# Kernel optimization log

Hardware: AMD Instinct MI355X
Metric: run time of the kernel (lower is better)

The kernel has to match this reference:

```python
import jax, jax.numpy as jnp
import numpy as np

K_SIZE = 3
SCALE = 4
PADDING = K_SIZE // 2


def setup_inputs() -> dict:
    key = jax.random.key(0)
    k1, k2, k3, k4 = jax.random.split(key, 4)
    B, C, H, W = 8, 3, 1024, 1024
    ho, wo = H // SCALE, W // SCALE
    img = jax.random.normal(k1, (B, C, H, W), dtype=jnp.float32)
    kernels = jax.random.uniform(k2, (B, K_SIZE * K_SIZE, ho, wo), dtype=jnp.float32)
    offsets_h = jax.random.normal(k3, (B, K_SIZE * K_SIZE, ho, wo), dtype=jnp.float32)
    offsets_v = jax.random.normal(k4, (B, K_SIZE * K_SIZE, ho, wo), dtype=jnp.float32)
    offset_unit = jnp.full((1,), 4.0, dtype=jnp.float32)
    return {"img": img, "kernels": kernels, "offsets_h": offsets_h,
            "offsets_v": offsets_v, "offset_unit": offset_unit}


def _adaptive_downsample(img, kernels, offsets_h, offsets_v, offset_unit):
    # img: [B,C,H,W]; kernels/offsets: [B,k^2,ho,wo]; offset_unit: [1]
    B, C, H, W = img.shape
    ho, wo = kernels.shape[2], kernels.shape[3]
    # reflection pad as in nn.ReflectionPad2d(padding)
    imgp = jnp.pad(img, ((0, 0), (0, 0), (PADDING, PADDING), (PADDING, PADDING)), mode="reflect")
    Hp, Wp = imgp.shape[2], imgp.shape[3]

    k = jnp.arange(K_SIZE)
    ky = jnp.repeat(k, K_SIZE).astype(jnp.float32)  # [k^2] row index of kernel tap
    kx = jnp.tile(k, K_SIZE).astype(jnp.float32)    # [k^2] col index of kernel tap

    # output-pixel centers in original image coords; +PADDING shift into padded
    # coords cancels the -PADDING tap centering, so padded sample position is
    # center + k (k in 0..k_size-1).
    cy = (jnp.arange(ho, dtype=jnp.float32) + 0.5) * SCALE - 0.5  # [ho]
    cx = (jnp.arange(wo, dtype=jnp.float32) + 0.5) * SCALE - 0.5  # [wo]

    ou = offset_unit.reshape(())
    # sample positions in padded image, shape [B, k^2, ho, wo]
    p_y = cy[None, None, :, None] + ky[None, :, None, None] + offsets_v * ou
    p_x = cx[None, None, None, :] + kx[None, :, None, None] + offsets_h * ou

    y0f = jnp.floor(p_y)
    x0f = jnp.floor(p_x)
    beta = p_y - y0f   # vertical bilinear weight
    alpha = p_x - x0f  # horizontal bilinear weight

    y0 = jnp.clip(y0f.astype(jnp.int32), 0, Hp - 1)
    y1 = jnp.clip(y0 + 1, 0, Hp - 1)
    x0 = jnp.clip(x0f.astype(jnp.int32), 0, Wp - 1)
    x1 = jnp.clip(x0 + 1, 0, Wp - 1)

    def gather(yi, xi):
        # imgp: [B,C,Hp,Wp]; yi/xi: [B,k^2,ho,wo] -> [B,C,k^2,ho,wo]
        return jax.vmap(lambda im, y, x: im[:, y, x])(imgp, yi, xi)

    v00 = gather(y0, x0)
    v01 = gather(y0, x1)
    v10 = gather(y1, x0)
    v11 = gather(y1, x1)

    a = alpha[:, None]  # [B,1,k^2,ho,wo]
    b_ = beta[:, None]
    val = ((1 - a) * (1 - b_) * v00 + a * (1 - b_) * v01 +
           (1 - a) * b_ * v10 + a * b_ * v11)  # [B,C,k^2,ho,wo]

    # per-pixel learned kernel weighted sum over the k^2 taps
    out = jnp.einsum("bckhw,bkhw->bchw", val, kernels)
    return out


def reference(img, kernels, offsets_h, offsets_v, offset_unit):
    return _adaptive_downsample(img, kernels, offsets_h, offsets_v, offset_unit)
```

## Files before the change

### kernel.cpp

```cpp
#include <hip/hip_runtime.h>
#include <cstdint>

namespace {
constexpr int B = 8, C = 3, H = 1024, W = 1024;
constexpr int HO = 256, WO = 256, K2 = 9;
constexpr int HP = H + 2, WP = W + 2;
constexpr int HW = H * W, HOWO = HO * WO;

constexpr int TW = 32, TH = 16;
constexpr int NTX = WO / TW;
constexpr int NTY = HO / TH;
constexpr int NT  = NTX * NTY;
constexpr int OF = 12;
constexpr int WINW = 4 * TW + 2 * OF;
constexpr int WINH = 4 * TH + 2 * OF;
constexpr int WPX  = WINW * WINH;
constexpr int CPR  = WINW / 4;
constexpr int CHPP = CPR * WINH;

constexpr size_t LA_BYTES  = (size_t)(WPX + 2) * 8;
constexpr size_t LDS_BYTES = LA_BYTES + (size_t)(WPX + 1) * 4;

__device__ __forceinline__ int reflect_src(int p, int n) {
    int s = p - 1;
    s = (s < 0) ? -s : s;
    s = (s >= n) ? (2 * n - 2 - s) : s;
    return s;
}

__global__ __launch_bounds__(512) void ds_fused(
    const float* __restrict__ img,
    const float* __restrict__ kern,
    const float* __restrict__ offh,
    const float* __restrict__ offv,
    const float* __restrict__ ou_p,
    float* __restrict__ out) {
    extern __shared__ unsigned char smem[];
    float2* __restrict__ lA = (float2*)smem;
    float*  __restrict__ lB = (float*)(smem + LA_BYTES);

    const int b   = blockIdx.x & 7;
    const int t   = blockIdx.x >> 3;
    const int tid = threadIdx.x;
    const int w0  = (t & (NTX - 1)) * TW;
    const int h0  = (t >> 3) * TH;
    const int X0  = 4 * w0 - (OF - 1);
    const int Y0  = 4 * h0 - (OF - 1);

    const float* __restrict__ p0 = img + (size_t)b * (C * HW);
    const float* __restrict__ p1 = p0 + HW;
    const float* __restrict__ p2 = p1 + HW;

    const int lw = tid & (TW - 1);
    const int lh = tid >> 5;
    const int h = h0 + lh, w = w0 + lw;
    const int pb = (b * K2) * HOWO + h * WO + w;
    float kv[K2], vv[K2], hh[K2];
#pragma unroll
    for (int k = 0; k < K2; ++k) {
        kv[k] = kern[pb + k * HOWO];
        vv[k] = offv[pb + k * HOWO];
        hh[k] = offh[pb + k * HOWO];
    }
    const float ou = ou_p[0];

    for (int i = tid; i < CHPP; i += 512) {
        int yy = i / CPR, xc = i - yy * CPR;
        int Yp = min(max(Y0 + yy, 0), HP - 1);
        int sy = reflect_src(Yp, H);
        int gx = X0 - 1 + 4 * xc;
        float4 a0, a1;
        if (gx >= 0 && gx <= W - 4) {
            a0 = *(const float4*)(p0 + (size_t)sy * W + gx);
            a1 = *(const float4*)(p1 + (size_t)sy * W + gx);
        } else {
            float t0[4], t1[4];
#pragma unroll
            for (int j = 0; j < 4; ++j) {
                int Xp = min(max(X0 + 4 * xc + j, 0), WP - 1);
                int sx = reflect_src(Xp, W);
                t0[j] = p0[(size_t)sy * W + sx];
                t1[j] = p1[(size_t)sy * W + sx];
            }
            a0 = make_float4(t0[0], t0[1], t0[2], t0[3]);
            a1 = make_float4(t1[0], t1[1], t1[2], t1[3]);
        }
        float4* dst = (float4*)(lA + 4 * i);
        dst[0] = make_float4(a0.x, a1.x, a0.y, a1.y);
        dst[1] = make_float4(a0.z, a1.z, a0.w, a1.w);
    }
    for (int i = tid; i < CHPP; i += 512) {
        int yy = i / CPR, xc = i - yy * CPR;
        int Yp = min(max(Y0 + yy, 0), HP - 1);
        int sy = reflect_src(Yp, H);
        int gx = X0 - 1 + 4 * xc;
        float4 a2;
        if (gx >= 0 && gx <= W - 4) {
            a2 = *(const float4*)(p2 + (size_t)sy * W + gx);
        } else {
            float t2[4];
#pragma unroll
            for (int j = 0; j < 4; ++j) {
                int Xp = min(max(X0 + 4 * xc + j, 0), WP - 1);
                int sx = reflect_src(Xp, W);
                t2[j] = p2[(size_t)sy * W + sx];
            }
            a2 = make_float4(t2[0], t2[1], t2[2], t2[3]);
        }
        *(float4*)(lB + 4 * i) = a2;
    }
    __syncthreads();

    const float cy = (h + 0.5f) * 4.0f - 0.5f;
    const float cx = (w + 0.5f) * 4.0f - 0.5f;
    float acc0 = 0.f, acc1 = 0.f, acc2 = 0.f;

#pragma unroll
    for (int k = 0; k < K2; ++k) {
        float py = cy + (float)(k / 3) + vv[k] * ou;
        float px = cx + (float)(k % 3) + hh[k] * ou;

        float y0f = floorf(py), x0f = floorf(px);
        float bb = py - y0f;
        float aa = px - x0f;

        int y0 = min(max((int)y0f, 0), HP - 1);
        int x0 = min(max((int)x0f, 0), WP - 1);
        int y1 = min(y0 + 1, HP - 1);
        int x1 = min(x0 + 1, WP - 1);

        float v00x, v00y, v00z, v01x, v01y, v01z;
        float v10x, v10y, v10z, v11x, v11y, v11z;

        bool inw = (y0 >= Y0) & (y1 <= Y0 + WINH - 1) &
                   (x0 >= X0) & (x1 <= X0 + WINW - 1);
        if (__builtin_expect(inw, 1)) {
            int i00 = (y0 - Y0) * WINW + (x0 - X0);
            int i10 = i00 + (y1 - y0) * WINW;
            bool dx = (x1 > x0);
            float2 a00 = lA[i00], a01 = lA[i00 + 1];
            float2 a10 = lA[i10], a11 = lA[i10 + 1];
            float  b00 = lB[i00], b01 = lB[i00 + 1];
            float  b10 = lB[i10], b11 = lB[i10 + 1];
            float2 s01 = dx ? a01 : a00;
            float2 s11 = dx ? a11 : a10;
            float  c01 = dx ? b01 : b00;
            float  c11 = dx ? b11 : b10;
            v00x = a00.x; v00y = a00.y; v00z = b00;
            v01x = s01.x; v01y = s01.y; v01z = c01;
            v10x = a10.x; v10y = a10.y; v10z = b10;
            v11x = s11.x; v11y = s11.y; v11z = c11;
        } else {
            int sy0 = reflect_src(y0, H), sy1 = reflect_src(y1, H);
            int sx0 = reflect_src(x0, W), sx1 = reflect_src(x1, W);
            size_t i0 = (size_t)sy0 * W + sx0, i1 = (size_t)sy0 * W + sx1;
            size_t i2 = (size_t)sy1 * W + sx0, i3 = (size_t)sy1 * W + sx1;
            v00x = p0[i0]; v01x = p0[i1]; v10x = p0[i2]; v11x = p0[i3];
            v00y = p1[i0]; v01y = p1[i1]; v10y = p1[i2]; v11y = p1[i3];
            v00z = p2[i0]; v01z = p2[i1]; v10z = p2[i2]; v11z = p2[i3];
        }

        float tx_, tu_;
        tx_ = v00x + aa * (v01x - v00x);
        tu_ = v10x + aa * (v11x - v10x);
        acc0 += kv[k] * (tx_ + bb * (tu_ - tx_));
        tx_ = v00y + aa * (v01y - v00y);
        tu_ = v10y + aa * (v11y - v10y);
        acc1 += kv[k] * (tx_ + bb * (tu_ - tx_));
        tx_ = v00z + aa * (v01z - v00z);
        tu_ = v10z + aa * (v11z - v10z);
        acc2 += kv[k] * (tx_ + bb * (tu_ - tx_));
    }

    size_t obase = ((size_t)b * C) * (size_t)HOWO + (size_t)h * WO + w;
    out[obase] = acc0;
    out[obase + (size_t)HOWO] = acc1;
    out[obase + (size_t)(2 * HOWO)] = acc2;
}
}

extern "C" void kernel_launch(void* const* d_in, const int* in_sizes, int n_in,
                              void* d_out, int out_size, void* d_ws, size_t ws_size,
                              hipStream_t stream) {
    const float* img  = (const float*)d_in[0];
    const float* kern = (const float*)d_in[1];
    const float* offh = (const float*)d_in[2];
    const float* offv = (const float*)d_in[3];
    const float* ou   = (const float*)d_in[4];
    float* out = (float*)d_out;

    static bool attr_set = false;
    if (!attr_set) {
        hipFuncSetAttribute(reinterpret_cast<const void*>(&ds_fused),
                            hipFuncAttributeMaxDynamicSharedMemorySize,
                            (int)LDS_BYTES);
        attr_set = true;
    }

    hipLaunchKernelGGL(ds_fused, dim3(B * NT), dim3(512), LDS_BYTES, stream,
                       img, kern, offh, offv, ou, out);
}
```

Before: 221.7 us.

## Stage image window into LDS with direct global-to-LDS DMA loads

```diff
diff --git a/kernel.cpp b/kernel.cpp
--- a/kernel.cpp
+++ b/kernel.cpp
@@ -17,9 +17,7 @@
 constexpr int WPX  = WINW * WINH;
 constexpr int CPR  = WINW / 4;
 constexpr int CHPP = CPR * WINH;
-
-constexpr size_t LA_BYTES  = (size_t)(WPX + 2) * 8;
-constexpr size_t LDS_BYTES = LA_BYTES + (size_t)(WPX + 1) * 4;
+constexpr size_t LDS_BYTES = (size_t)WPX * 12;
 
 __device__ __forceinline__ int reflect_src(int p, int n) {
     int s = p - 1;
@@ -28,16 +26,24 @@
     return s;
 }
 
-__global__ __launch_bounds__(512) void ds_fused(
+__device__ __forceinline__ void dma16(const float* g, float* l) {
+    __builtin_amdgcn_global_load_lds(
+        (const __attribute__((address_space(1))) unsigned int*)g,
+        (__attribute__((address_space(3))) unsigned int*)l,
+        16, 0, 0);
+}
+
+__global__ __launch_bounds__(512) void ds_dma(
     const float* __restrict__ img,
     const float* __restrict__ kern,
     const float* __restrict__ offh,
     const float* __restrict__ offv,
     const float* __restrict__ ou_p,
     float* __restrict__ out) {
-    extern __shared__ unsigned char smem[];
-    float2* __restrict__ lA = (float2*)smem;
-    float*  __restrict__ lB = (float*)(smem + LA_BYTES);
+    extern __shared__ __align__(16) float smem[];
+    float* __restrict__ win0 = smem;
+    float* __restrict__ win1 = smem + WPX;
+    float* __restrict__ win2 = smem + 2 * WPX;
 
     const int b   = blockIdx.x & 7;
     const int t   = blockIdx.x >> 3;
@@ -65,51 +71,39 @@
     const float ou = ou_p[0];
 
     for (int i = tid; i < CHPP; i += 512) {
-        int yy = i / CPR, xc = i - yy * CPR;
+        int yy = i / CPR;
+        int xc = i - yy * CPR;
         int Yp = min(max(Y0 + yy, 0), HP - 1);
         int sy = reflect_src(Yp, H);
         int gx = X0 - 1 + 4 * xc;
-        float4 a0, a1;
-        if (gx >= 0 && gx <= W - 4) {
-            a0 = *(const float4*)(p0 + (size_t)sy * W + gx);
-            a1 = *(const float4*)(p1 + (size_t)sy * W + gx);
-        } else {
-            float t0[4], t1[4];
-#pragma unroll
-            for (int j = 0; j < 4; ++j) {
-                int Xp = min(max(X0 + 4 * xc + j, 0), WP - 1);
-                int sx = reflect_src(Xp, W);
-                t0[j] = p0[(size_t)sy * W + sx];
-                t1[j] = p1[(size_t)sy * W + sx];
-            }
-            a0 = make_float4(t0[0], t0[1], t0[2], t0[3]);
-            a1 = make_float4(t1[0], t1[1], t1[2], t1[3]);
-        }
-        float4* dst = (float4*)(lA + 4 * i);
-        dst[0] = make_float4(a0.x, a1.x, a0.y, a1.y);
-        dst[1] = make_float4(a0.z, a1.z, a0.w, a1.w);
-    }
-    for (int i = tid; i < CHPP; i += 512) {
-        int yy = i / CPR, xc = i - yy * CPR;
-        int Yp = min(max(Y0 + yy, 0), HP - 1);
-        int sy = reflect_src(Yp, H);
-        int gx = X0 - 1 + 4 * xc;
-        float4 a2;
-        if (gx >= 0 && gx <= W - 4) {
-            a2 = *(const float4*)(p2 + (size_t)sy * W + gx);
-        } else {
-            float t2[4];
-#pragma unroll
-            for (int j = 0; j < 4; ++j) {
-                int Xp = min(max(X0 + 4 * xc + j, 0), WP - 1);
-                int sx = reflect_src(Xp, W);
-                t2[j] = p2[(size_t)sy * W + sx];
-            }
-            a2 = make_float4(t2[0], t2[1], t2[2], t2[3]);
-        }
-        *(float4*)(lB + 4 * i) = a2;
+        gx = min(max(gx, 0), W - 4);
+        const size_t si = (size_t)sy * W + gx;
+        const int lbase = (i & ~63) * 4;
+        dma16(p0 + si, win0 + lbase);
+        dma16(p1 + si, win1 + lbase);
+        dma16(p2 + si, win2 + lbase);
     }
     __syncthreads();
+
+    const bool ledge = (X0 - 1 < 0);
+    const bool redge = (X0 - 1 + 4 * (CPR - 1) > W - 4);
+    if (ledge | redge) {
+        const int xbase = ledge ? 0 : (WINW - 12);
+        for (int i = tid; i < 12 * WINH; i += 512) {
+            int r = i / 12, cc = i - r * 12;
+            int xx = xbase + cc;
+            int Yp = min(max(Y0 + r, 0), HP - 1);
+            int sy = reflect_src(Yp, H);
+            int Xp = min(max(X0 + xx, 0), WP - 1);
+            int sx = reflect_src(Xp, W);
+            size_t si = (size_t)sy * W + sx;
+            int wi = r * WINW + xx;
+            win0[wi] = p0[si];
+            win1[wi] = p1[si];
+            win2[wi] = p2[si];
+        }
+        __syncthreads();
+    }
 
     const float cy = (h + 0.5f) * 4.0f - 0.5f;
     const float cx = (w + 0.5f) * 4.0f - 0.5f;
@@ -138,18 +132,18 @@
             int i00 = (y0 - Y0) * WINW + (x0 - X0);
             int i10 = i00 + (y1 - y0) * WINW;
             bool dx = (x1 > x0);
-            float2 a00 = lA[i00], a01 = lA[i00 + 1];
-            float2 a10 = lA[i10], a11 = lA[i10 + 1];
-            float  b00 = lB[i00], b01 = lB[i00 + 1];
-            float  b10 = lB[i10], b11 = lB[i10 + 1];
-            float2 s01 = dx ? a01 : a00;
-            float2 s11 = dx ? a11 : a10;
-            float  c01 = dx ? b01 : b00;
-            float  c11 = dx ? b11 : b10;
-            v00x = a00.x; v00y = a00.y; v00z = b00;
-            v01x = s01.x; v01y = s01.y; v01z = c01;
-            v10x = a10.x; v10y = a10.y; v10z = b10;
-            v11x = s11.x; v11y = s11.y; v11z = c11;
+            float a00 = win0[i00], a01 = win0[i00 + 1];
+            float a10 = win0[i10], a11 = win0[i10 + 1];
+            float b00 = win1[i00], b01 = win1[i00 + 1];
+            float b10 = win1[i10], b11 = win1[i10 + 1];
+            float c00 = win2[i00], c01 = win2[i00 + 1];
+            float c10 = win2[i10], c11 = win2[i10 + 1];
+            v00x = a00; v01x = dx ? a01 : a00;
+            v10x = a10; v11x = dx ? a11 : a10;
+            v00y = b00; v01y = dx ? b01 : b00;
+            v10y = b10; v11y = dx ? b11 : b10;
+            v00z = c00; v01z = dx ? c01 : c00;
+            v10z = c10; v11z = dx ? c11 : c10;
         } else {
             int sy0 = reflect_src(y0, H), sy1 = reflect_src(y1, H);
             int sx0 = reflect_src(x0, W), sx1 = reflect_src(x1, W);
@@ -191,12 +185,12 @@
 
     static bool attr_set = false;
     if (!attr_set) {
-        hipFuncSetAttribute(reinterpret_cast<const void*>(&ds_fused),
+        hipFuncSetAttribute(reinterpret_cast<const void*>(&ds_dma),
                             hipFuncAttributeMaxDynamicSharedMemorySize,
                             (int)LDS_BYTES);
         attr_set = true;
     }
 
-    hipLaunchKernelGGL(ds_fused, dim3(B * NT), dim3(512), LDS_BYTES, stream,
+    hipLaunchKernelGGL(ds_dma, dim3(B * NT), dim3(512), LDS_BYTES, stream,
                        img, kern, offh, offv, ou, out);
 }
```

Result: faster. 209.5 us (-5.5%).
